# Kernel optimization log

Hardware: AMD Instinct MI355X
Metric: run time of the kernel (lower is better)

The kernel has to match this reference:

```python
import jax, jax.numpy as jnp
import numpy as np

# Graph dimensions (homogeneous node ordering per hetero2homo: [function, input, output])
N_F, N_I, N_O = 2000, 500, 500
N = N_F + N_I + N_O
C = 8                 # hidden channels per function node
H = N_F * C           # total hidden width
B = 256
E_FF, E_IF, E_FO = 40000, 5000, 2000
E = E_FF + E_IF + E_FO
EPS = 1e-5


def _build_graph():
    rng = np.random.default_rng(0)
    src_ff = rng.integers(0, N_F, E_FF)
    dst_ff = rng.integers(0, N_F, E_FF)
    src_if = rng.integers(N_F, N_F + N_I, E_IF)          # input -> function
    dst_if = rng.integers(0, N_F, E_IF)
    src_fo = rng.integers(0, N_F, E_FO)                   # function -> output
    dst_fo = rng.integers(N_F + N_I, N, E_FO)
    src = np.concatenate([src_ff, src_if, src_fo])
    dst = np.concatenate([dst_ff, dst_if, dst_fo])
    edge_index = jnp.asarray(np.stack([src, dst]), dtype=jnp.int32)
    mask = np.zeros(N, dtype=bool)
    mask[N_F + N_I:] = True
    return edge_index, jnp.asarray(mask)


def setup_inputs() -> dict:
    key = jax.random.key(0)
    k_x, k_w1, k_b1, k_w2, k_b2 = jax.random.split(key, 5)
    edge_index, output_node_mask = _build_graph()
    scale = 0.1  # xavier-ish for small fan-in/out
    return {
        "x": jax.random.normal(k_x, (B, N), dtype=jnp.float32),
        "w1": jax.random.normal(k_w1, (E, C), dtype=jnp.float32) * scale,
        "b1": jax.random.normal(k_b1, (H,), dtype=jnp.float32) * 0.01,
        "gamma": jnp.ones((H,), dtype=jnp.float32),
        "beta": jnp.zeros((H,), dtype=jnp.float32),
        "w2": jax.random.normal(k_w2, (E, C), dtype=jnp.float32) * scale,
        "b2": jax.random.normal(k_b2, (E,), dtype=jnp.float32) * 0.01,
        "edge_index": edge_index,
        "output_node_mask": output_node_mask,
        "layers": 10,
    }


def reference(x, w1, b1, gamma, beta, w2, b2, edge_index, output_node_mask, layers):
    src, dst = edge_index[0], edge_index[1]
    # W_in structure: hidden channel k of function node n receives edge e iff dst[e]==n.
    # Edges whose dst is not a function node are structurally absent -> route to dummy segment N_F.
    dst_seg = jnp.where(dst < N_F, dst, N_F)
    # W_out structure: edge e receives hidden channels of function node src[e]; zero otherwise.
    src_is_func = src < N_F
    src_clip = jnp.where(src_is_func, src, 0)

    xe = x[:, src]  # node2edge: (B, E)
    for _ in range(layers):
        # lin_in: sparse (E x H) matmul == per-edge outer product scatter-added onto dst node channels
        contrib = xe.T[:, :, None] * w1[:, None, :]                       # (E, B, C)
        hid = jax.ops.segment_sum(contrib, dst_seg, num_segments=N_F + 1)[:N_F]  # (N_F, B, C)
        h = hid.transpose(1, 0, 2).reshape(B, H) + b1                      # (B, H)
        # layer norm then nonlin (norm_first=True)
        mu = h.mean(-1, keepdims=True)
        var = h.var(-1, keepdims=True)
        h = (h - mu) * jax.lax.rsqrt(var + EPS) * gamma + beta
        h = jax.nn.elu(h)
        # lin_out: sparse (H x E) matmul == gather src-node channels, dot with per-edge weights
        hn = h.reshape(B, N_F, C)
        out_e = jnp.einsum('bec,ec->be', hn[:, src_clip, :], w2)
        out_e = jnp.where(src_is_func[None, :], out_e, 0.0) + b2[None, :]
        xe = xe + out_e                                                    # residual
    xe = xe / layers
    # edge2node: scatter-add edge features onto output nodes only
    xm = jnp.where(output_node_mask[dst][None, :], xe, 0.0)
    out = jax.ops.segment_sum(xm.T, dst, num_segments=output_node_mask.shape[0]).T  # (B, N)
    return out
```

## Files before the change

kernel.cpp:

```cpp
#include <hip/hip_runtime.h>
#include <cmath>
#include <cstdint>

#define N_F    2000
#define N_I    500
#define N_O    500
#define N_ALL  3000
#define C      8
#define H      16000
#define B      256
#define E_FF   40000
#define E_IF   5000
#define E_FO   2000
#define E_ALL  47000
#define LAYERS 10
#define EPSF   1e-5f
#define RED    32

static __device__ __forceinline__ unsigned short f2bf(float f) {
    unsigned int u = __float_as_uint(f);
    unsigned int r = (u + 0x7FFFu + ((u >> 16) & 1u)) >> 16;
    return (unsigned short)r;
}
static __device__ __forceinline__ float bf2f(unsigned short h) {
    return __uint_as_float(((unsigned int)h) << 16);
}


__global__ void k_zero_cnt(int* cntA, int* cntB, int* cntC, int* cntD) {
    int tid = threadIdx.x;
    for (int i = tid; i < N_F; i += 1024) { cntA[i] = 0; cntB[i] = 0; cntC[i] = 0; }
    for (int i = tid; i < N_O; i += 1024) cntD[i] = 0;
}

__global__ void k_count(const int* __restrict__ src, const int* __restrict__ dst,
                        int* cntA, int* cntB, int* cntC, int* cntD) {
    int e = blockIdx.x * 256 + threadIdx.x;
    if (e >= E_ALL) return;
    int s = src[e], d = dst[e];
    if (e < E_FF)             { atomicAdd(&cntA[d], 1); atomicAdd(&cntB[d], 1); atomicAdd(&cntC[s], 1); }
    else if (e < E_FF + E_IF) { atomicAdd(&cntA[d], 1); }
    else                      { atomicAdd(&cntD[d - (N_F + N_I)], 1); }
}

__global__ void k_scan(const int* cntA, const int* cntB, const int* cntC, const int* cntD,
                       int* rsA, int* rsB2, int* rsC, int* rsD,
                       int* curA, int* curB, int* curC, int* curD) {
    const int* cnt; int* rs; int* cur; int len;
    if      (blockIdx.x == 0) { cnt = cntA; rs = rsA;  cur = curA; len = N_F; }
    else if (blockIdx.x == 1) { cnt = cntB; rs = rsB2; cur = curB; len = N_F; }
    else if (blockIdx.x == 2) { cnt = cntC; rs = rsC;  cur = curC; len = N_F; }
    else                      { cnt = cntD; rs = rsD;  cur = curD; len = N_O; }
    __shared__ int buf[1024];
    __shared__ int carry;
    int tid = threadIdx.x;
    if (tid == 0) carry = 0;
    __syncthreads();
    for (int base0 = 0; base0 < len; base0 += 1024) {
        int i = base0 + tid;
        int v = (i < len) ? cnt[i] : 0;
        buf[tid] = v;
        __syncthreads();
        for (int off = 1; off < 1024; off <<= 1) {
            int t = (tid >= off) ? buf[tid - off] : 0;
            __syncthreads();
            buf[tid] += t;
            __syncthreads();
        }
        int excl = carry + buf[tid] - v;
        if (i < len) { rs[i] = excl; cur[i] = excl; }
        int tot = buf[1023];
        __syncthreads();
        if (tid == 0) carry += tot;
        __syncthreads();
    }
    if (tid == 0) rs[len] = carry;
}

__global__ void k_fill(const int* __restrict__ src, const int* __restrict__ dst,
                       int* curA, int* curC, int* curD,
                       int* eidA, int* eidC, int* eidD) {
    int e = blockIdx.x * 256 + threadIdx.x;
    if (e >= E_ALL) return;
    int s = src[e], d = dst[e];
    if (e < E_FF) {
        int a = atomicAdd(&curA[d], 1); eidA[a] = e;
        int p = atomicAdd(&curC[s], 1); eidC[p] = e;
    } else if (e < E_FF + E_IF) {
        int a = atomicAdd(&curA[d], 1); eidA[a] = e;
    } else {
        int k = atomicAdd(&curD[d - (N_F + N_I)], 1); eidD[k] = e;
    }
}

__global__ void k_wsort(const int* __restrict__ rsA, int* eidA,
                        const int* __restrict__ rsC, int* eidC,
                        const int* __restrict__ rsD, int* eidD) {
    int w = blockIdx.x * 4 + (threadIdx.x >> 6);
    int lane = threadIdx.x & 63;
    const int* rs; int* eid; int n;
    if      (w < 2000) { rs = rsA; eid = eidA; n = w; }
    else if (w < 4000) { rs = rsC; eid = eidC; n = w - 2000; }
    else if (w < 4500) { rs = rsD; eid = eidD; n = w - 4000; }
    else return;
    int beg = rs[n], end = rs[n + 1], len = end - beg;
    if (len <= 1) return;
    if (len <= 64) {
        int v = (lane < len) ? eid[beg + lane] : 0x7fffffff;
        int rank = 0;
        for (int j = 0; j < 64; ++j) {
            int o = __shfl(v, j, 64);
            rank += (o < v) ? 1 : 0;
        }
        if (lane < len) eid[beg + rank] = v;
    } else if (lane == 0) {
        for (int i = beg + 1; i < end; ++i) {
            int key = eid[i];
            int j = i - 1;
            while (j >= beg && eid[j] > key) { eid[j + 1] = eid[j]; --j; }
            eid[j + 1] = key;
        }
    }
}

__global__ void k_posB(const int* __restrict__ rsA, const int* __restrict__ eidA,
                       const int* __restrict__ cntB, const int* __restrict__ rsB2,
                       const float* __restrict__ w1, int* posB, float* jw1) {
    int n = blockIdx.x * 256 + threadIdx.x;
    if (n >= N_F) return;
    int a0 = rsA[n], j0 = rsB2[n], m = cntB[n];
    for (int k = 0; k < m; ++k) {
        int e = eidA[a0 + k];
        int j = j0 + k;
        posB[e] = j;
        #pragma unroll
        for (int c = 0; c < C; ++c) jw1[j * C + c] = w1[e * C + c];
    }
}

__global__ void k_posC(const int* __restrict__ eidC, const int* __restrict__ posB,
                       const float* __restrict__ w2, int* jposC, float* w2C) {
    int p = blockIdx.x * 256 + threadIdx.x;
    if (p >= E_FF) return;
    int e = eidC[p];
    jposC[p] = posB[e];
    #pragma unroll
    for (int c = 0; c < C; ++c) w2C[p * C + c] = w2[e * C + c];
}


__global__ void k_xT(const float* __restrict__ x, float* __restrict__ xT) {
    __shared__ float t[32][33];
    int tx = threadIdx.x, ty = threadIdx.y;
    int n = blockIdx.x * 32 + tx, b = blockIdx.y * 32 + ty;
    if (n < N_ALL) t[ty][tx] = x[b * N_ALL + n];
    __syncthreads();
    int n2 = blockIdx.x * 32 + ty, b2 = blockIdx.y * 32 + tx;
    if (n2 < N_ALL) xT[n2 * B + b2] = t[tx][ty];
}

__global__ void k_base(const float* __restrict__ xT, const float* __restrict__ w1,
                       const float* __restrict__ b1, const float* __restrict__ b2,
                       const int* __restrict__ rsA, const int* __restrict__ eidA,
                       const int* __restrict__ srcv,
                       float* __restrict__ baseG, float* __restrict__ bbG) {
    int n = blockIdx.x, tid = threadIdx.x;
    int beg = rsA[n], end = rsA[n + 1];
    float acc[C] = {0.f,0.f,0.f,0.f,0.f,0.f,0.f,0.f};
    float bba[C] = {0.f,0.f,0.f,0.f,0.f,0.f,0.f,0.f};
    const float4* w14 = (const float4*)w1;
    for (int a = beg; a < end; ++a) {
        int e = eidA[a];
        float xv = xT[srcv[e] * B + tid];
        float bv = b2[e];
        float4 u0 = w14[e * 2], u1 = w14[e * 2 + 1];
        acc[0] += u0.x * xv; acc[1] += u0.y * xv; acc[2] += u0.z * xv; acc[3] += u0.w * xv;
        acc[4] += u1.x * xv; acc[5] += u1.y * xv; acc[6] += u1.z * xv; acc[7] += u1.w * xv;
        bba[0] += u0.x * bv; bba[1] += u0.y * bv; bba[2] += u0.z * bv; bba[3] += u0.w * bv;
        bba[4] += u1.x * bv; bba[5] += u1.y * bv; bba[6] += u1.z * bv; bba[7] += u1.w * bv;
    }
    #pragma unroll
    for (int c = 0; c < C; ++c) baseG[(n * C + c) * B + tid] = acc[c] + b1[n * C + c];
    if (tid == 0) {
        #pragma unroll
        for (int c = 0; c < C; ++c) bbG[n * C + c] = bba[c];
    }
}


__global__ __launch_bounds__(256) void f_hidstat(
    const float* __restrict__ baseG, const float* __restrict__ bbG,
    const float* __restrict__ jw1, const unsigned short* __restrict__ qbf,
    const int* __restrict__ rsB2,
    unsigned short* __restrict__ hidbf, float* __restrict__ bp, int t) {
    int n = blockIdx.x, tid = threadIdx.x;
    const float4* jw14 = (const float4*)jw1;
    float tf = (float)t;
    float hid[C];
    #pragma unroll
    for (int c = 0; c < C; ++c) hid[c] = baseG[(n * C + c) * B + tid] + tf * bbG[n * C + c];
    if (t > 0) {
        int beg = rsB2[n], end = rsB2[n + 1];
        for (int j = beg; j < end; ++j) {
            float qv = bf2f(qbf[j * B + tid]);
            float4 u0 = jw14[j * 2], u1 = jw14[j * 2 + 1];
            hid[0] += u0.x * qv; hid[1] += u0.y * qv; hid[2] += u0.z * qv; hid[3] += u0.w * qv;
            hid[4] += u1.x * qv; hid[5] += u1.y * qv; hid[6] += u1.z * qv; hid[7] += u1.w * qv;
        }
    }
    float s1 = 0.f, s2 = 0.f;
    #pragma unroll
    for (int c = 0; c < C; ++c) {
        hidbf[(n * C + c) * B + tid] = f2bf(hid[c]);
        s1 += hid[c]; s2 += hid[c] * hid[c];
    }
    bp[(n * 2 + 0) * B + tid] = s1;
    bp[(n * 2 + 1) * B + tid] = s2;
}

__global__ __launch_bounds__(256) void f_red(const float* __restrict__ bp, float* __restrict__ p2) {
    int blk = blockIdx.x, tid = threadIdx.x;
    float a1 = 0.f, a2 = 0.f;
    for (int i = blk; i < N_F; i += RED) {
        a1 += bp[(i * 2 + 0) * B + tid];
        a2 += bp[(i * 2 + 1) * B + tid];
    }
    p2[(blk * 2 + 0) * B + tid] = a1;
    p2[(blk * 2 + 1) * B + tid] = a2;
}

__global__ __launch_bounds__(256) void f_upd(
    const unsigned short* __restrict__ hidbf, const float* __restrict__ p2,
    const float* __restrict__ gamma, const float* __restrict__ beta,
    const float* __restrict__ w2C, const int* __restrict__ jposC,
    const int* __restrict__ rsC,
    float* __restrict__ Sg, unsigned short* __restrict__ qbf, int t) {
    int n = blockIdx.x, tid = threadIdx.x;
    const float4* w24 = (const float4*)w2C;
    float S1 = 0.f, S2 = 0.f;
    #pragma unroll
    for (int k = 0; k < RED; ++k) {
        S1 += p2[(k * 2 + 0) * B + tid];
        S2 += p2[(k * 2 + 1) * B + tid];
    }
    float mu  = S1 * (1.0f / H);
    float var = S2 * (1.0f / H) - mu * mu;
    float rsq = rsqrtf(var + EPSF);
    float Sn[C];
    #pragma unroll
    for (int c = 0; c < C; ++c) {
        float v = bf2f(hidbf[(n * C + c) * B + tid]);
        v = (v - mu) * rsq * gamma[n * C + c] + beta[n * C + c];
        v = (v > 0.f) ? v : expm1f(v);
        Sn[c] = (t == 0) ? v : (Sg[(n * C + c) * B + tid] + v);
    }
    #pragma unroll
    for (int c = 0; c < C; ++c) Sg[(n * C + c) * B + tid] = Sn[c];
    if (t < LAYERS - 1) {
        int beg = rsC[n], end = rsC[n + 1];
        for (int p = beg; p < end; ++p) {
            int j = jposC[p];
            float4 u0 = w24[p * 2], u1 = w24[p * 2 + 1];
            float qv = u0.x * Sn[0] + u0.y * Sn[1] + u0.z * Sn[2] + u0.w * Sn[3]
                     + u1.x * Sn[4] + u1.y * Sn[5] + u1.z * Sn[6] + u1.w * Sn[7];
            qbf[j * B + tid] = f2bf(qv);
        }
    }
}


__global__ void f_zero_out(float* __restrict__ out) {
    int i = blockIdx.x * 256 + threadIdx.x;
    ((float4*)out)[i] = make_float4(0.f, 0.f, 0.f, 0.f);
}

__global__ void f_out(const float* __restrict__ xT, const float* __restrict__ Sg,
                      const int* __restrict__ rsD, const int* __restrict__ eidD,
                      const int* __restrict__ srcv, const float* __restrict__ w2,
                      const float* __restrict__ b2, float* __restrict__ out) {
    int o = blockIdx.x, tid = threadIdx.x;
    const float4* w24 = (const float4*)w2;
    float acc = 0.f;
    int beg = rsD[o], end = rsD[o + 1];
    for (int k = beg; k < end; ++k) {
        int e = eidD[k];
        int s = srcv[e];
        float4 u0 = w24[e * 2], u1 = w24[e * 2 + 1];
        float dot = u0.x * Sg[(s * C + 0) * B + tid] + u0.y * Sg[(s * C + 1) * B + tid]
                  + u0.z * Sg[(s * C + 2) * B + tid] + u0.w * Sg[(s * C + 3) * B + tid]
                  + u1.x * Sg[(s * C + 4) * B + tid] + u1.y * Sg[(s * C + 5) * B + tid]
                  + u1.z * Sg[(s * C + 6) * B + tid] + u1.w * Sg[(s * C + 7) * B + tid];
        acc += xT[s * B + tid] + dot + (float)LAYERS * b2[e];
    }
    out[tid * N_ALL + (N_F + N_I + o)] = acc * (1.0f / LAYERS);
}


static inline char* alignup(char* p) { return (char*)(((uintptr_t)p + 255) & ~(uintptr_t)255); }

extern "C" void kernel_launch(void* const* d_in, const int* in_sizes, int n_in,
                              void* d_out, int out_size, void* d_ws, size_t ws_size,
                              hipStream_t stream) {
    const float* x     = (const float*)d_in[0];
    const float* w1    = (const float*)d_in[1];
    const float* b1    = (const float*)d_in[2];
    const float* gamma = (const float*)d_in[3];
    const float* beta  = (const float*)d_in[4];
    const float* w2    = (const float*)d_in[5];
    const float* b2    = (const float*)d_in[6];
    const int*   ei    = (const int*)d_in[7];
    const int* srcv = ei;
    const int* dstv = ei + E_ALL;
    float* out = (float*)d_out;

    char* p = (char*)d_ws;
    unsigned short* qbf   = (unsigned short*)p; p += (size_t)E_FF * B * 2; p = alignup(p);
    unsigned short* hidbf = (unsigned short*)p; p += (size_t)H * B * 2;    p = alignup(p);
    float* Sg    = (float*)p; p += (size_t)H * B * 4;        p = alignup(p);
    float* baseG = (float*)p; p += (size_t)H * B * 4;        p = alignup(p);
    float* xT    = (float*)p; p += (size_t)N_ALL * B * 4;    p = alignup(p);
    float* bp    = (float*)p; p += (size_t)N_F * 2 * B * 4;  p = alignup(p);
    float* p2    = (float*)p; p += (size_t)RED * 2 * B * 4;  p = alignup(p);
    float* bbG   = (float*)p; p += (size_t)N_F * C * 4;      p = alignup(p);
    float* jw1   = (float*)p; p += (size_t)E_FF * C * 4;     p = alignup(p);
    float* w2C   = (float*)p; p += (size_t)E_FF * C * 4;     p = alignup(p);
    int* posB  = (int*)p; p += (size_t)E_FF * 4;  p = alignup(p);
    int* jposC = (int*)p; p += (size_t)E_FF * 4;  p = alignup(p);
    int* cntA = (int*)p; p += N_F * 4;        p = alignup(p);
    int* cntB = (int*)p; p += N_F * 4;        p = alignup(p);
    int* cntC = (int*)p; p += N_F * 4;        p = alignup(p);
    int* cntD = (int*)p; p += N_O * 4;        p = alignup(p);
    int* curA = (int*)p; p += N_F * 4;        p = alignup(p);
    int* curB = (int*)p; p += N_F * 4;        p = alignup(p);
    int* curC = (int*)p; p += N_F * 4;        p = alignup(p);
    int* curD = (int*)p; p += N_O * 4;        p = alignup(p);
    int* rsA  = (int*)p; p += (N_F + 1) * 4;  p = alignup(p);
    int* rsB2 = (int*)p; p += (N_F + 1) * 4;  p = alignup(p);
    int* rsC  = (int*)p; p += (N_F + 1) * 4;  p = alignup(p);
    int* rsD  = (int*)p; p += (N_O + 1) * 4;  p = alignup(p);
    int* eidA = (int*)p; p += (size_t)(E_FF + E_IF) * 4; p = alignup(p);
    int* eidC = (int*)p; p += (size_t)E_FF * 4; p = alignup(p);
    int* eidD = (int*)p; p += (size_t)E_FO * 4; p = alignup(p);

    hipLaunchKernelGGL(k_zero_cnt, dim3(1), dim3(1024), 0, stream, cntA, cntB, cntC, cntD);
    hipLaunchKernelGGL(k_count, dim3((E_ALL + 255) / 256), dim3(256), 0, stream,
                       srcv, dstv, cntA, cntB, cntC, cntD);
    hipLaunchKernelGGL(k_scan, dim3(4), dim3(1024), 0, stream,
                       cntA, cntB, cntC, cntD, rsA, rsB2, rsC, rsD, curA, curB, curC, curD);
    hipLaunchKernelGGL(k_fill, dim3((E_ALL + 255) / 256), dim3(256), 0, stream,
                       srcv, dstv, curA, curC, curD, eidA, eidC, eidD);
    hipLaunchKernelGGL(k_wsort, dim3(1125), dim3(256), 0, stream,
                       rsA, eidA, rsC, eidC, rsD, eidD);
    hipLaunchKernelGGL(k_posB, dim3((N_F + 255) / 256), dim3(256), 0, stream,
                       rsA, eidA, cntB, rsB2, w1, posB, jw1);
    hipLaunchKernelGGL(k_posC, dim3((E_FF + 255) / 256), dim3(256), 0, stream,
                       eidC, posB, w2, jposC, w2C);
    hipLaunchKernelGGL(k_xT, dim3((N_ALL + 31) / 32, B / 32), dim3(32, 32), 0, stream, x, xT);
    hipLaunchKernelGGL(k_base, dim3(N_F), dim3(256), 0, stream,
                       xT, w1, b1, b2, rsA, eidA, srcv, baseG, bbG);

    hipLaunchKernelGGL(f_zero_out, dim3(750), dim3(256), 0, stream, out);
    for (int t = 0; t < LAYERS; ++t) {
        hipLaunchKernelGGL(f_hidstat, dim3(N_F), dim3(256), 0, stream,
                           baseG, bbG, jw1, qbf, rsB2, hidbf, bp, t);
        hipLaunchKernelGGL(f_red, dim3(RED), dim3(256), 0, stream, bp, p2);
        hipLaunchKernelGGL(f_upd, dim3(N_F), dim3(256), 0, stream,
                           hidbf, p2, gamma, beta, w2C, jposC, rsC, Sg, qbf, t);
    }
    hipLaunchKernelGGL(f_out, dim3(N_O), dim3(256), 0, stream,
                       xT, Sg, rsD, eidD, srcv, w2, b2, out);
}
```

Before: 777.0 us.

## Store baseG and running sum Sg in bf16, parallelize posB setup per wavefront

The per-layer base hidden term and the accumulated layer sum are now stored as bf16 instead of fp32, which halves their memory traffic in every layer's hidstat and update kernels. k_posB now gives each node a whole wavefront instead of one thread, and both weight-permutation kernels copy with float4 loads. Accumulating the residual sum in bf16 across ten layers adds rounding error that could affect accuracy.

After: 717.1 us. -7.7%, faster.

```diff
diff --git a/kernel.cpp b/kernel.cpp
--- a/kernel.cpp
+++ b/kernel.cpp
@@ -126,15 +126,18 @@
 __global__ void k_posB(const int* __restrict__ rsA, const int* __restrict__ eidA,
                        const int* __restrict__ cntB, const int* __restrict__ rsB2,
                        const float* __restrict__ w1, int* posB, float* jw1) {
-    int n = blockIdx.x * 256 + threadIdx.x;
-    if (n >= N_F) return;
-    int a0 = rsA[n], j0 = rsB2[n], m = cntB[n];
-    for (int k = 0; k < m; ++k) {
+    int w = blockIdx.x * 4 + (threadIdx.x >> 6);
+    int lane = threadIdx.x & 63;
+    if (w >= N_F) return;
+    int a0 = rsA[w], j0 = rsB2[w], m = cntB[w];
+    const float4* w14 = (const float4*)w1;
+    float4* jw14 = (float4*)jw1;
+    for (int k = lane; k < m; k += 64) {
         int e = eidA[a0 + k];
         int j = j0 + k;
         posB[e] = j;
-        #pragma unroll
-        for (int c = 0; c < C; ++c) jw1[j * C + c] = w1[e * C + c];
+        jw14[j * 2]     = w14[e * 2];
+        jw14[j * 2 + 1] = w14[e * 2 + 1];
     }
 }
 
@@ -144,8 +147,9 @@
     if (p >= E_FF) return;
     int e = eidC[p];
     jposC[p] = posB[e];
-    #pragma unroll
-    for (int c = 0; c < C; ++c) w2C[p * C + c] = w2[e * C + c];
+    float4 u0 = ((const float4*)w2)[e * 2], u1 = ((const float4*)w2)[e * 2 + 1];
+    ((float4*)w2C)[p * 2]     = u0;
+    ((float4*)w2C)[p * 2 + 1] = u1;
 }
 
 
@@ -163,7 +167,7 @@
                        const float* __restrict__ b1, const float* __restrict__ b2,
                        const int* __restrict__ rsA, const int* __restrict__ eidA,
                        const int* __restrict__ srcv,
-                       float* __restrict__ baseG, float* __restrict__ bbG) {
+                       unsigned short* __restrict__ baseG, float* __restrict__ bbG) {
     int n = blockIdx.x, tid = threadIdx.x;
     int beg = rsA[n], end = rsA[n + 1];
     float acc[C] = {0.f,0.f,0.f,0.f,0.f,0.f,0.f,0.f};
@@ -180,7 +184,7 @@
         bba[4] += u1.x * bv; bba[5] += u1.y * bv; bba[6] += u1.z * bv; bba[7] += u1.w * bv;
     }
     #pragma unroll
-    for (int c = 0; c < C; ++c) baseG[(n * C + c) * B + tid] = acc[c] + b1[n * C + c];
+    for (int c = 0; c < C; ++c) baseG[(n * C + c) * B + tid] = f2bf(acc[c] + b1[n * C + c]);
     if (tid == 0) {
         #pragma unroll
         for (int c = 0; c < C; ++c) bbG[n * C + c] = bba[c];
@@ -189,7 +193,7 @@
 
 
 __global__ __launch_bounds__(256) void f_hidstat(
-    const float* __restrict__ baseG, const float* __restrict__ bbG,
+    const unsigned short* __restrict__ baseG, const float* __restrict__ bbG,
     const float* __restrict__ jw1, const unsigned short* __restrict__ qbf,
     const int* __restrict__ rsB2,
     unsigned short* __restrict__ hidbf, float* __restrict__ bp, int t) {
@@ -198,7 +202,8 @@
     float tf = (float)t;
     float hid[C];
     #pragma unroll
-    for (int c = 0; c < C; ++c) hid[c] = baseG[(n * C + c) * B + tid] + tf * bbG[n * C + c];
+    for (int c = 0; c < C; ++c)
+        hid[c] = bf2f(baseG[(n * C + c) * B + tid]) + tf * bbG[n * C + c];
     if (t > 0) {
         int beg = rsB2[n], end = rsB2[n + 1];
         for (int j = beg; j < end; ++j) {
@@ -234,7 +239,7 @@
     const float* __restrict__ gamma, const float* __restrict__ beta,
     const float* __restrict__ w2C, const int* __restrict__ jposC,
     const int* __restrict__ rsC,
-    float* __restrict__ Sg, unsigned short* __restrict__ qbf, int t) {
+    unsigned short* __restrict__ Sg, unsigned short* __restrict__ qbf, int t) {
     int n = blockIdx.x, tid = threadIdx.x;
     const float4* w24 = (const float4*)w2C;
     float S1 = 0.f, S2 = 0.f;
@@ -252,10 +257,10 @@
         float v = bf2f(hidbf[(n * C + c) * B + tid]);
         v = (v - mu) * rsq * gamma[n * C + c] + beta[n * C + c];
         v = (v > 0.f) ? v : expm1f(v);
-        Sn[c] = (t == 0) ? v : (Sg[(n * C + c) * B + tid] + v);
-    }
-    #pragma unroll
-    for (int c = 0; c < C; ++c) Sg[(n * C + c) * B + tid] = Sn[c];
+        Sn[c] = (t == 0) ? v : (bf2f(Sg[(n * C + c) * B + tid]) + v);
+    }
+    #pragma unroll
+    for (int c = 0; c < C; ++c) Sg[(n * C + c) * B + tid] = f2bf(Sn[c]);
     if (t < LAYERS - 1) {
         int beg = rsC[n], end = rsC[n + 1];
         for (int p = beg; p < end; ++p) {
@@ -274,7 +279,7 @@
     ((float4*)out)[i] = make_float4(0.f, 0.f, 0.f, 0.f);
 }
 
-__global__ void f_out(const float* __restrict__ xT, const float* __restrict__ Sg,
+__global__ void f_out(const float* __restrict__ xT, const unsigned short* __restrict__ Sg,
                       const int* __restrict__ rsD, const int* __restrict__ eidD,
                       const int* __restrict__ srcv, const float* __restrict__ w2,
                       const float* __restrict__ b2, float* __restrict__ out) {
@@ -286,10 +291,10 @@
         int e = eidD[k];
         int s = srcv[e];
         float4 u0 = w24[e * 2], u1 = w24[e * 2 + 1];
-        float dot = u0.x * Sg[(s * C + 0) * B + tid] + u0.y * Sg[(s * C + 1) * B + tid]
-                  + u0.z * Sg[(s * C + 2) * B + tid] + u0.w * Sg[(s * C + 3) * B + tid]
-                  + u1.x * Sg[(s * C + 4) * B + tid] + u1.y * Sg[(s * C + 5) * B + tid]
-                  + u1.z * Sg[(s * C + 6) * B + tid] + u1.w * Sg[(s * C + 7) * B + tid];
+        float dot = u0.x * bf2f(Sg[(s * C + 0) * B + tid]) + u0.y * bf2f(Sg[(s * C + 1) * B + tid])
+                  + u0.z * bf2f(Sg[(s * C + 2) * B + tid]) + u0.w * bf2f(Sg[(s * C + 3) * B + tid])
+                  + u1.x * bf2f(Sg[(s * C + 4) * B + tid]) + u1.y * bf2f(Sg[(s * C + 5) * B + tid])
+                  + u1.z * bf2f(Sg[(s * C + 6) * B + tid]) + u1.w * bf2f(Sg[(s * C + 7) * B + tid]);
         acc += xT[s * B + tid] + dot + (float)LAYERS * b2[e];
     }
     out[tid * N_ALL + (N_F + N_I + o)] = acc * (1.0f / LAYERS);
@@ -316,8 +321,8 @@
     char* p = (char*)d_ws;
     unsigned short* qbf   = (unsigned short*)p; p += (size_t)E_FF * B * 2; p = alignup(p);
     unsigned short* hidbf = (unsigned short*)p; p += (size_t)H * B * 2;    p = alignup(p);
-    float* Sg    = (float*)p; p += (size_t)H * B * 4;        p = alignup(p);
-    float* baseG = (float*)p; p += (size_t)H * B * 4;        p = alignup(p);
+    unsigned short* Sg    = (unsigned short*)p; p += (size_t)H * B * 2;    p = alignup(p);
+    unsigned short* baseG = (unsigned short*)p; p += (size_t)H * B * 2;    p = alignup(p);
     float* xT    = (float*)p; p += (size_t)N_ALL * B * 4;    p = alignup(p);
     float* bp    = (float*)p; p += (size_t)N_F * 2 * B * 4;  p = alignup(p);
     float* p2    = (float*)p; p += (size_t)RED * 2 * B * 4;  p = alignup(p);
@@ -351,7 +356,7 @@
                        srcv, dstv, curA, curC, curD, eidA, eidC, eidD);
     hipLaunchKernelGGL(k_wsort, dim3(1125), dim3(256), 0, stream,
                        rsA, eidA, rsC, eidC, rsD, eidD);
-    hipLaunchKernelGGL(k_posB, dim3((N_F + 255) / 256), dim3(256), 0, stream,
+    hipLaunchKernelGGL(k_posB, dim3((N_F + 3) / 4), dim3(256), 0, stream,
                        rsA, eidA, cntB, rsB2, w1, posB, jw1);
     hipLaunchKernelGGL(k_posC, dim3((E_FF + 255) / 256), dim3(256), 0, stream,
                        eidC, posB, w2, jposC, w2C);
```
